# Kernel optimization log

Hardware: AMD Instinct MI355X
Metric: run time of the kernel (lower is better)

The kernel has to match this reference:

```python
import jax, jax.numpy as jnp
import numpy as np

D_MODEL = 1024
N_HEADS = 16
DEPTH = D_MODEL // N_HEADS
NEG_INF = -1.0e9


def setup_inputs() -> dict:
    key = jax.random.key(0)
    ks = jax.random.split(key, 11)
    B, S = 2, 2048
    xk = jax.random.normal(ks[0], (B, S, D_MODEL), jnp.float32)
    xq = jax.random.normal(ks[1], (B, S, D_MODEL), jnp.float32)
    xv = jax.random.normal(ks[2], (B, S, D_MODEL), jnp.float32)
    sc = 1.0 / np.sqrt(D_MODEL)
    wq = jax.random.normal(ks[3], (D_MODEL, D_MODEL), jnp.float32) * sc
    wk = jax.random.normal(ks[4], (D_MODEL, D_MODEL), jnp.float32) * sc
    wv = jax.random.normal(ks[5], (D_MODEL, D_MODEL), jnp.float32) * sc
    wo = jax.random.normal(ks[6], (D_MODEL, D_MODEL), jnp.float32) * sc
    bq = jnp.zeros((D_MODEL,), jnp.float32)
    bk = jnp.zeros((D_MODEL,), jnp.float32)
    bv = jnp.zeros((D_MODEL,), jnp.float32)
    bo = jnp.zeros((D_MODEL,), jnp.float32)
    return {"xk": xk, "xq": xq, "xv": xv, "wq": wq, "bq": bq, "wk": wk,
            "bk": bk, "wv": wv, "bv": bv, "wo": wo, "bo": bo}


def _split_heads(t):
    # [B, S, D] -> [B, H, S, depth]
    B, S, _ = t.shape
    return t.reshape(B, S, N_HEADS, DEPTH).transpose(0, 2, 1, 3)


def reference(xk, xq, xv, wq, bq, wk, bk, wv, bv, wo, bo):
    B, Sq, _ = xq.shape
    Sk = xk.shape[1]
    q = _split_heads(xq @ wq + bq)  # [B,H,Sq,d]
    k = _split_heads(xk @ wk + bk)  # [B,H,Sk,d]
    v = _split_heads(xv @ wv + bv)  # [B,H,Sk,d]
    logits = jnp.einsum('bhqd,bhkd->bhqk', q, k) / jnp.sqrt(
        jnp.asarray(DEPTH, q.dtype))
    # additive causal mask: (1 - lower_triangular) * -1e9
    causal = (1.0 - jnp.tril(jnp.ones((Sq, Sk), logits.dtype))) * NEG_INF
    logits = logits + causal[None, None, :, :]
    attn = jax.nn.softmax(logits, axis=-1)
    out = jnp.einsum('bhqk,bhkd->bhqd', attn, v)
    out = out.transpose(0, 2, 1, 3).reshape(B, Sq, D_MODEL)
    return out @ wo + bo
```

## Files before the change

### kernel.cpp

```cpp
#include <hip/hip_runtime.h>

typedef unsigned short u16;
typedef unsigned int u32;
typedef u16 u16x8 __attribute__((ext_vector_type(8)));
typedef u32 u32x2 __attribute__((ext_vector_type(2)));
typedef __bf16 bf16x8 __attribute__((ext_vector_type(8)));
typedef float f32x4 __attribute__((ext_vector_type(4)));

#define DM 1024
#define SEQ 2048
#define BATCH 2
#define MROWS 4096

__device__ __forceinline__ u16 f2bf(float f) {
  unsigned int x = __builtin_bit_cast(unsigned int, f);
  x += 0x7fffu + ((x >> 16) & 1u);
  return (u16)(x >> 16);
}

__device__ __forceinline__ u32 pack2bf(float lo, float hi) {
  return __builtin_amdgcn_perm(__builtin_bit_cast(u32, hi),
                               __builtin_bit_cast(u32, lo), 0x07060302u);
}

__device__ __forceinline__ void gld16(const void* g, void* l) {
  __builtin_amdgcn_global_load_lds(
      (const __attribute__((address_space(1))) void*)g,
      (__attribute__((address_space(3))) void*)l, 16, 0, 0);
}

struct TrArgs { const float* in[4]; u16* out[4]; };

__global__ __launch_bounds__(256) void transpose_w4(TrArgs a) {
  const float* __restrict__ in = a.in[blockIdx.z];
  u16* __restrict__ out = a.out[blockIdx.z];
  __shared__ u16 T[64][72];
  int r0 = blockIdx.y * 64, c0 = blockIdx.x * 64;
  int t = threadIdx.x;
  int r = t >> 3, cg = (t & 7) * 8;
#pragma unroll
  for (int p = 0; p < 2; p++) {
    const float* src = in + (size_t)(r0 + r + p * 32) * DM + c0 + cg;
    f32x4 x0 = *(const f32x4*)src;
    f32x4 x1 = *(const f32x4*)(src + 4);
    u16x8 v;
#pragma unroll
    for (int j = 0; j < 4; j++) { v[j] = f2bf(x0[j]); v[4 + j] = f2bf(x1[j]); }
    *(u16x8*)(&T[r + p * 32][cg]) = v;
  }
  __syncthreads();
#pragma unroll
  for (int p = 0; p < 2; p++) {
    int orow = r + p * 32;
    u16x8 v;
#pragma unroll
    for (int j = 0; j < 8; j++) v[j] = T[cg + j][orow];
    *(u16x8*)(out + (size_t)(c0 + orow) * DM + r0 + cg) = v;
  }
}

struct CastArgs { const float* in[3]; u16* out[3]; };

__global__ __launch_bounds__(256) void cast_x(CastArgs a) {
  const float* __restrict__ in = a.in[blockIdx.y];
  u16* __restrict__ out = a.out[blockIdx.y];
  size_t e = ((size_t)blockIdx.x * 256 + threadIdx.x) * 8;
  f32x4 a0 = *(const f32x4*)(in + e);
  f32x4 a1 = *(const f32x4*)(in + e + 4);
  u16x8 v;
#pragma unroll
  for (int j = 0; j < 4; j++) { v[j] = f2bf(a0[j]); v[4 + j] = f2bf(a1[j]); }
  *(u16x8*)(out + e) = v;
}

struct GemmArgs { const void* A[3]; const u16* WT[3]; const float* bias[3]; void* C[3]; };

template <int MT, int NT, int BK, bool AF32, bool OF32, bool VT>
__global__ __launch_bounds__(256) void gemmT(GemmArgs g) {
  constexpr int CH = BK / 8;
  constexpr int CM = CH - 1;
  constexpr int SH = (CH == 4) ? 1 : 0;
  __shared__ __align__(16) u16 As[MT * 32 * BK];
  __shared__ __align__(16) u16 Bs[NT * 32 * BK];
  const int z = blockIdx.z;
  const u16* __restrict__ WT = g.WT[z];
  const int tid = threadIdx.x, lane = tid & 63, wave = tid >> 6;
  const int fr = lane & 15, kq = lane >> 4;
  const int mq = (wave >> 1) * (MT * 16), nq = (wave & 1) * (NT * 16);
  const int m0 = blockIdx.y * (MT * 32), n0 = blockIdx.x * (NT * 32);
  const int fsel = (fr >> SH) & CM;
  f32x4 acc[MT][NT] = {};

  for (int kk = 0; kk < DM; kk += BK) {
    __syncthreads();
    constexpr int AI = MT * 32 * CH / 256;
    constexpr int BI = NT * 32 * CH / 256;
    if constexpr (AF32) {
      const float* A = (const float*)g.A[z];
#pragma unroll
      for (int i = 0; i < AI; i++) {
        int ci = i * 256 + tid, row = ci / CH, sl = ci % CH;
        int sc = (sl ^ ((row >> SH) & CM)) * 8;
        const float* s0 = A + (size_t)(m0 + row) * DM + kk + sc;
        f32x4 a0 = *(const f32x4*)s0, a1 = *(const f32x4*)(s0 + 4);
        u16x8 v;
#pragma unroll
        for (int j = 0; j < 4; j++) { v[j] = f2bf(a0[j]); v[4 + j] = f2bf(a1[j]); }
        *(u16x8*)(As + ci * 8) = v;
      }
    } else {
      const u16* A = (const u16*)g.A[z];
#pragma unroll
      for (int i = 0; i < AI; i++) {
        int ci = i * 256 + tid, row = ci / CH, sl = ci % CH;
        int sc = (sl ^ ((row >> SH) & CM)) * 8;
        gld16(A + (size_t)(m0 + row) * DM + kk + sc, As + ci * 8);
      }
    }
#pragma unroll
    for (int i = 0; i < BI; i++) {
      int ci = i * 256 + tid, row = ci / CH, sl = ci % CH;
      int sc = (sl ^ ((row >> SH) & CM)) * 8;
      gld16(WT + (size_t)(n0 + row) * DM + kk + sc, Bs + ci * 8);
    }
    __syncthreads();
#pragma unroll
    for (int kc = 0; kc < BK / 32; kc++) {
      bf16x8 af[MT], bfr[NT];
      const int fo = ((kc * 4 + kq) ^ fsel) * 8;
#pragma unroll
      for (int mt = 0; mt < MT; mt++)
        af[mt] = __builtin_bit_cast(
            bf16x8, *(const u16x8*)(As + (mq + mt * 16 + fr) * BK + fo));
#pragma unroll
      for (int nt = 0; nt < NT; nt++)
        bfr[nt] = __builtin_bit_cast(
            bf16x8, *(const u16x8*)(Bs + (nq + nt * 16 + fr) * BK + fo));
#pragma unroll
      for (int mt = 0; mt < MT; mt++)
#pragma unroll
        for (int nt = 0; nt < NT; nt++)
          acc[mt][nt] = __builtin_amdgcn_mfma_f32_16x16x32_bf16(
              af[mt], bfr[nt], acc[mt][nt], 0, 0, 0);
    }
  }
  const float* __restrict__ bias = g.bias[z];
  const bool vtr = VT && (z == 2);
#pragma unroll
  for (int nt = 0; nt < NT; nt++) {
    int col = n0 + nq + nt * 16 + fr;
    float bb = bias[col];
#pragma unroll
    for (int mt = 0; mt < MT; mt++)
#pragma unroll
      for (int r = 0; r < 4; r++) {
        int row = m0 + mq + mt * 16 + kq * 4 + r;
        float val = acc[mt][nt][r] + bb;
        if constexpr (OF32) {
          ((float*)g.C[z])[(size_t)row * DM + col] = val;
        } else {
          u16* C = (u16*)g.C[z];
          if (vtr) {
            size_t idx = ((size_t)((row >> 11) * 16 + (col >> 6)) * 64 +
                          (col & 63)) * SEQ + (row & 2047);
            C[idx] = f2bf(val);
          } else {
            C[(size_t)row * DM + col] = f2bf(val);
          }
        }
      }
  }
}

__global__ __launch_bounds__(128) void attn4(u16* __restrict__ Q,
                                             const u16* __restrict__ K,
                                             const u16* __restrict__ Vtg) {
  __shared__ __align__(16) u16 Ksh[64 * 64];
  __shared__ __align__(16) u16 Vsh[64 * 64];
  __shared__ __align__(16) u16 Psh[64 * 64];
  __shared__ float Lbuf[2][32];
  const int tid = threadIdx.x, wq = tid >> 6, lane = tid & 63;
  const int fr = lane & 15, kq = lane >> 4, f7 = fr & 7;
  const int bh = blockIdx.x, b = bh >> 4, h = bh & 15;
  const int qt = 31 - blockIdx.y;
  const float C1 = 0.125f * 1.44269504f;

  int xo[2];
  xo[0] = (kq ^ f7) * 8;
  xo[1] = ((4 + kq) ^ f7) * 8;

  const u16* kp[4];
  const u16* vp[4];
#pragma unroll
  for (int i = 0; i < 4; i++) {
    int ci = i * 128 + tid, row = ci >> 3, sl = ci & 7;
    int sc = (sl ^ (row & 7)) * 8;
    kp[i] = K + (size_t)(b * SEQ + row) * DM + h * 64 + sc;
    vp[i] = Vtg + (size_t)(bh * 64 + row) * SEQ + sc;
  }

  bf16x8 qf[2][2];
#pragma unroll
  for (int qtl = 0; qtl < 2; qtl++) {
    size_t qr = (size_t)(b * SEQ + qt * 64 + wq * 32 + qtl * 16 + fr) * DM + h * 64;
#pragma unroll
    for (int kk = 0; kk < 2; kk++)
      qf[qtl][kk] =
          __builtin_bit_cast(bf16x8, *(const u16x8*)(Q + qr + kk * 32 + kq * 8));
  }

  f32x4 ov[2][4] = {};
  float lac[2] = {0.f, 0.f};

  for (int t = 0; t <= qt; t++) {
    __syncthreads();
#pragma unroll
    for (int i = 0; i < 4; i++) {
      int ci = i * 128 + tid;
      gld16(kp[i] + (size_t)t * 64 * DM, Ksh + ci * 8);
      gld16(vp[i] + t * 64, Vsh + ci * 8);
    }
    __syncthreads();

    f32x4 st[2][4];
#pragma unroll
    for (int kt = 0; kt < 4; kt++) {
      bf16x8 k0 = __builtin_bit_cast(
          bf16x8, *(const u16x8*)(Ksh + (kt * 16 + fr) * 64 + xo[0]));
      bf16x8 k1 = __builtin_bit_cast(
          bf16x8, *(const u16x8*)(Ksh + (kt * 16 + fr) * 64 + xo[1]));
#pragma unroll
      for (int qtl = 0; qtl < 2; qtl++) {
        f32x4 s = {};
        s = __builtin_amdgcn_mfma_f32_16x16x32_bf16(k0, qf[qtl][0], s, 0, 0, 0);
        s = __builtin_amdgcn_mfma_f32_16x16x32_bf16(k1, qf[qtl][1], s, 0, 0, 0);
        st[qtl][kt] = s;
      }
    }
    if (t == qt) {
#pragma unroll
      for (int qtl = 0; qtl < 2; qtl++)
#pragma unroll
        for (int kt = 0; kt < 4; kt++)
#pragma unroll
          for (int r = 0; r < 4; r++)
            if (kt * 16 + kq * 4 + r > wq * 32 + qtl * 16 + fr)
              st[qtl][kt][r] = -1e30f;
    }
#pragma unroll
    for (int qtl = 0; qtl < 2; qtl++) {
      float ls = 0.f;
      int prow = (wq * 32 + qtl * 16 + fr) * 64;
#pragma unroll
      for (int kt = 0; kt < 4; kt++) {
        float p0 = __builtin_amdgcn_exp2f(st[qtl][kt][0] * C1);
        float p1 = __builtin_amdgcn_exp2f(st[qtl][kt][1] * C1);
        float p2 = __builtin_amdgcn_exp2f(st[qtl][kt][2] * C1);
        float p3 = __builtin_amdgcn_exp2f(st[qtl][kt][3] * C1);
        ls += (p0 + p1) + (p2 + p3);
        u32x2 d;
        d[0] = pack2bf(p0, p1);
        d[1] = pack2bf(p2, p3);
        int sl = (2 * kt + (kq >> 1)) ^ f7;
        *(u32x2*)(Psh + prow + sl * 8 + (kq & 1) * 4) = d;
      }
      ls += __shfl_xor(ls, 16);
      ls += __shfl_xor(ls, 32);
      lac[qtl] += ls;
    }
#pragma unroll
    for (int kk = 0; kk < 2; kk++) {
      bf16x8 pa[2];
#pragma unroll
      for (int qtl = 0; qtl < 2; qtl++)
        pa[qtl] = __builtin_bit_cast(
            bf16x8,
            *(const u16x8*)(Psh + (wq * 32 + qtl * 16 + fr) * 64 + xo[kk]));
#pragma unroll
      for (int nt = 0; nt < 4; nt++) {
        bf16x8 vb = __builtin_bit_cast(
            bf16x8, *(const u16x8*)(Vsh + (nt * 16 + fr) * 64 + xo[kk]));
#pragma unroll
        for (int qtl = 0; qtl < 2; qtl++)
          ov[qtl][nt] = __builtin_amdgcn_mfma_f32_16x16x32_bf16(
              pa[qtl], vb, ov[qtl][nt], 0, 0, 0);
      }
    }
  }
  if (kq == 0) {
    Lbuf[wq][fr] = lac[0];
    Lbuf[wq][16 + fr] = lac[1];
  }
#pragma unroll
  for (int qtl = 0; qtl < 2; qtl++) {
    float rinv[4];
#pragma unroll
    for (int r = 0; r < 4; r++)
      rinv[r] = 1.0f / Lbuf[wq][qtl * 16 + kq * 4 + r];
#pragma unroll
    for (int nt = 0; nt < 4; nt++)
#pragma unroll
      for (int r = 0; r < 4; r++) {
        int row = qt * 64 + wq * 32 + qtl * 16 + kq * 4 + r;
        Q[(size_t)(b * SEQ + row) * DM + h * 64 + nt * 16 + fr] =
            f2bf(ov[qtl][nt][r] * rinv[r]);
      }
  }
}

extern "C" void kernel_launch(void* const* d_in, const int* in_sizes, int n_in,
                              void* d_out, int out_size, void* d_ws,
                              size_t ws_size, hipStream_t stream) {
  const float* xk = (const float*)d_in[0];
  const float* xq = (const float*)d_in[1];
  const float* xv = (const float*)d_in[2];
  const float* wq = (const float*)d_in[3];
  const float* bq = (const float*)d_in[4];
  const float* wk = (const float*)d_in[5];
  const float* bk = (const float*)d_in[6];
  const float* wv = (const float*)d_in[7];
  const float* bv = (const float*)d_in[8];
  const float* wo = (const float*)d_in[9];
  const float* bo = (const float*)d_in[10];

  u16* Qb = (u16*)d_ws;
  u16* Kb = Qb + (size_t)MROWS * DM;
  u16* Vb = Kb + (size_t)MROWS * DM;
  u16* WTq = Vb + (size_t)MROWS * DM;
  u16* WTk = WTq + (size_t)DM * DM;
  u16* WTv = WTk + (size_t)DM * DM;
  u16* WTo = WTv + (size_t)DM * DM;
  u16* Xq = WTo + (size_t)DM * DM;
  u16* Xk = Xq + (size_t)MROWS * DM;
  u16* Xv = Xk + (size_t)MROWS * DM;
  const bool cast_path =
      ws_size >= ((size_t)(3 * 8 + 4 * 2 + 3 * 8)) * 1024 * 1024;

  dim3 blk(256);

  TrArgs tr;
  tr.in[0] = wq; tr.in[1] = wk; tr.in[2] = wv; tr.in[3] = wo;
  tr.out[0] = WTq; tr.out[1] = WTk; tr.out[2] = WTv; tr.out[3] = WTo;
  transpose_w4<<<dim3(16, 16, 4), blk, 0, stream>>>(tr);

  GemmArgs gq;
  gq.WT[0] = WTq; gq.WT[1] = WTk; gq.WT[2] = WTv;
  gq.bias[0] = bq; gq.bias[1] = bk; gq.bias[2] = bv;
  gq.C[0] = Qb; gq.C[1] = Kb; gq.C[2] = Vb;
  if (cast_path) {
    CastArgs ca;
    ca.in[0] = xq; ca.in[1] = xk; ca.in[2] = xv;
    ca.out[0] = Xq; ca.out[1] = Xk; ca.out[2] = Xv;
    cast_x<<<dim3(MROWS * DM / 2048, 3), blk, 0, stream>>>(ca);
    gq.A[0] = Xq; gq.A[1] = Xk; gq.A[2] = Xv;
    gemmT<4, 4, 64, false, false, true>
        <<<dim3(DM / 128, MROWS / 128, 3), blk, 0, stream>>>(gq);
  } else {
    gq.A[0] = xq; gq.A[1] = xk; gq.A[2] = xv;
    gemmT<4, 4, 64, true, false, true>
        <<<dim3(DM / 128, MROWS / 128, 3), blk, 0, stream>>>(gq);
  }

  attn4<<<dim3(BATCH * 16, 32), dim3(128), 0, stream>>>(Qb, Kb, Vb);

  GemmArgs go;
  go.A[0] = Qb; go.WT[0] = WTo; go.bias[0] = bo; go.C[0] = d_out;
  go.A[1] = Qb; go.WT[1] = WTo; go.bias[1] = bo; go.C[1] = d_out;
  go.A[2] = Qb; go.WT[2] = WTo; go.bias[2] = bo; go.C[2] = d_out;
  gemmT<2, 2, 64, false, true, false>
      <<<dim3(DM / 64, MROWS / 64, 1), blk, 0, stream>>>(go);
}
```

Before: 240.9 us.

## Double-buffer LDS in GEMM and attention, fuse input cast, widen out-proj tile

Both the projection GEMM and the attention kernel now use two LDS buffers, so the next K-step (or next K/V tile) is loaded while MFMAs run on the current one. Each iteration now needs only one barrier instead of two. The separate fp32-to-bf16 cast kernel is removed, and the QKV GEMM converts fp32 inputs directly while staging them. The transposed V store is packed into 8-byte writes, and the output projection moves to a 2x4 tile. The risks are the extra LDS use and a smaller K step (32), and the fp32 A staging stays synchronous, so less of its load latency can be hidden.

```diff
diff --git a/kernel.cpp b/kernel.cpp
--- a/kernel.cpp
+++ b/kernel.cpp
@@ -17,7 +17,9 @@
   x += 0x7fffu + ((x >> 16) & 1u);
   return (u16)(x >> 16);
 }
-
+__device__ __forceinline__ u32 f2bf2(float lo, float hi) {
+  return (u32)f2bf(lo) | ((u32)f2bf(hi) << 16);
+}
 __device__ __forceinline__ u32 pack2bf(float lo, float hi) {
   return __builtin_amdgcn_perm(__builtin_bit_cast(u32, hi),
                                __builtin_bit_cast(u32, lo), 0x07060302u);
@@ -59,91 +61,76 @@
   }
 }
 
-struct CastArgs { const float* in[3]; u16* out[3]; };
-
-__global__ __launch_bounds__(256) void cast_x(CastArgs a) {
-  const float* __restrict__ in = a.in[blockIdx.y];
-  u16* __restrict__ out = a.out[blockIdx.y];
-  size_t e = ((size_t)blockIdx.x * 256 + threadIdx.x) * 8;
-  f32x4 a0 = *(const f32x4*)(in + e);
-  f32x4 a1 = *(const f32x4*)(in + e + 4);
-  u16x8 v;
-#pragma unroll
-  for (int j = 0; j < 4; j++) { v[j] = f2bf(a0[j]); v[4 + j] = f2bf(a1[j]); }
-  *(u16x8*)(out + e) = v;
-}
-
 struct GemmArgs { const void* A[3]; const u16* WT[3]; const float* bias[3]; void* C[3]; };
 
-template <int MT, int NT, int BK, bool AF32, bool OF32, bool VT>
+template <int MT, int NT, bool AF32, bool OF32, bool VT>
 __global__ __launch_bounds__(256) void gemmT(GemmArgs g) {
-  constexpr int CH = BK / 8;
-  constexpr int CM = CH - 1;
-  constexpr int SH = (CH == 4) ? 1 : 0;
-  __shared__ __align__(16) u16 As[MT * 32 * BK];
-  __shared__ __align__(16) u16 Bs[NT * 32 * BK];
+  __shared__ __align__(16) u16 As[2][MT * 32 * 32];
+  __shared__ __align__(16) u16 Bs[2][NT * 32 * 32];
   const int z = blockIdx.z;
   const u16* __restrict__ WT = g.WT[z];
   const int tid = threadIdx.x, lane = tid & 63, wave = tid >> 6;
   const int fr = lane & 15, kq = lane >> 4;
   const int mq = (wave >> 1) * (MT * 16), nq = (wave & 1) * (NT * 16);
   const int m0 = blockIdx.y * (MT * 32), n0 = blockIdx.x * (NT * 32);
-  const int fsel = (fr >> SH) & CM;
+  const int fo = ((kq ^ ((fr >> 1) & 3)) * 8);
+  constexpr int AI = MT / 2, BI = NT / 2;
   f32x4 acc[MT][NT] = {};
 
-  for (int kk = 0; kk < DM; kk += BK) {
-    __syncthreads();
-    constexpr int AI = MT * 32 * CH / 256;
-    constexpr int BI = NT * 32 * CH / 256;
+  auto stage = [&](int buf, int kk) {
     if constexpr (AF32) {
       const float* A = (const float*)g.A[z];
 #pragma unroll
       for (int i = 0; i < AI; i++) {
-        int ci = i * 256 + tid, row = ci / CH, sl = ci % CH;
-        int sc = (sl ^ ((row >> SH) & CM)) * 8;
+        int ci = i * 256 + tid, row = ci >> 2, sl = ci & 3;
+        int sc = (sl ^ ((row >> 1) & 3)) * 8;
         const float* s0 = A + (size_t)(m0 + row) * DM + kk + sc;
         f32x4 a0 = *(const f32x4*)s0, a1 = *(const f32x4*)(s0 + 4);
         u16x8 v;
 #pragma unroll
         for (int j = 0; j < 4; j++) { v[j] = f2bf(a0[j]); v[4 + j] = f2bf(a1[j]); }
-        *(u16x8*)(As + ci * 8) = v;
+        *(u16x8*)(As[buf] + ci * 8) = v;
       }
     } else {
       const u16* A = (const u16*)g.A[z];
 #pragma unroll
       for (int i = 0; i < AI; i++) {
-        int ci = i * 256 + tid, row = ci / CH, sl = ci % CH;
-        int sc = (sl ^ ((row >> SH) & CM)) * 8;
-        gld16(A + (size_t)(m0 + row) * DM + kk + sc, As + ci * 8);
+        int ci = i * 256 + tid, row = ci >> 2, sl = ci & 3;
+        int sc = (sl ^ ((row >> 1) & 3)) * 8;
+        gld16(A + (size_t)(m0 + row) * DM + kk + sc, As[buf] + ci * 8);
       }
     }
 #pragma unroll
     for (int i = 0; i < BI; i++) {
-      int ci = i * 256 + tid, row = ci / CH, sl = ci % CH;
-      int sc = (sl ^ ((row >> SH) & CM)) * 8;
-      gld16(WT + (size_t)(n0 + row) * DM + kk + sc, Bs + ci * 8);
-    }
+      int ci = i * 256 + tid, row = ci >> 2, sl = ci & 3;
+      int sc = (sl ^ ((row >> 1) & 3)) * 8;
+      gld16(WT + (size_t)(n0 + row) * DM + kk + sc, Bs[buf] + ci * 8);
+    }
+  };
+
+  stage(0, 0);
+  __syncthreads();
+  for (int k = 0; k < DM / 32; k++) {
+    if (k + 1 < DM / 32) stage((k + 1) & 1, (k + 1) * 32);
+    const int buf = k & 1;
+    bf16x8 af[MT], bfr[NT];
+#pragma unroll
+    for (int mt = 0; mt < MT; mt++)
+      af[mt] = __builtin_bit_cast(
+          bf16x8, *(const u16x8*)(As[buf] + (mq + mt * 16 + fr) * 32 + fo));
+#pragma unroll
+    for (int nt = 0; nt < NT; nt++)
+      bfr[nt] = __builtin_bit_cast(
+          bf16x8, *(const u16x8*)(Bs[buf] + (nq + nt * 16 + fr) * 32 + fo));
+#pragma unroll
+    for (int mt = 0; mt < MT; mt++)
+#pragma unroll
+      for (int nt = 0; nt < NT; nt++)
+        acc[mt][nt] = __builtin_amdgcn_mfma_f32_16x16x32_bf16(
+            af[mt], bfr[nt], acc[mt][nt], 0, 0, 0);
     __syncthreads();
-#pragma unroll
-    for (int kc = 0; kc < BK / 32; kc++) {
-      bf16x8 af[MT], bfr[NT];
-      const int fo = ((kc * 4 + kq) ^ fsel) * 8;
-#pragma unroll
-      for (int mt = 0; mt < MT; mt++)
-        af[mt] = __builtin_bit_cast(
-            bf16x8, *(const u16x8*)(As + (mq + mt * 16 + fr) * BK + fo));
-#pragma unroll
-      for (int nt = 0; nt < NT; nt++)
-        bfr[nt] = __builtin_bit_cast(
-            bf16x8, *(const u16x8*)(Bs + (nq + nt * 16 + fr) * BK + fo));
-#pragma unroll
-      for (int mt = 0; mt < MT; mt++)
-#pragma unroll
-        for (int nt = 0; nt < NT; nt++)
-          acc[mt][nt] = __builtin_amdgcn_mfma_f32_16x16x32_bf16(
-              af[mt], bfr[nt], acc[mt][nt], 0, 0, 0);
-    }
-  }
+  }
+
   const float* __restrict__ bias = g.bias[z];
   const bool vtr = VT && (z == 2);
 #pragma unroll
@@ -151,32 +138,34 @@
     int col = n0 + nq + nt * 16 + fr;
     float bb = bias[col];
 #pragma unroll
-    for (int mt = 0; mt < MT; mt++)
-#pragma unroll
-      for (int r = 0; r < 4; r++) {
-        int row = m0 + mq + mt * 16 + kq * 4 + r;
-        float val = acc[mt][nt][r] + bb;
-        if constexpr (OF32) {
-          ((float*)g.C[z])[(size_t)row * DM + col] = val;
-        } else {
-          u16* C = (u16*)g.C[z];
-          if (vtr) {
-            size_t idx = ((size_t)((row >> 11) * 16 + (col >> 6)) * 64 +
-                          (col & 63)) * SEQ + (row & 2047);
-            C[idx] = f2bf(val);
-          } else {
-            C[(size_t)row * DM + col] = f2bf(val);
-          }
+    for (int mt = 0; mt < MT; mt++) {
+      int row0 = m0 + mq + mt * 16 + kq * 4;
+      if (vtr) {
+        u32x2 d;
+        d[0] = f2bf2(acc[mt][nt][0] + bb, acc[mt][nt][1] + bb);
+        d[1] = f2bf2(acc[mt][nt][2] + bb, acc[mt][nt][3] + bb);
+        size_t idx = ((size_t)((row0 >> 11) * 16 + (col >> 6)) * 64 +
+                      (col & 63)) * SEQ + (row0 & 2047);
+        *(u32x2*)((u16*)g.C[z] + idx) = d;
+      } else {
+#pragma unroll
+        for (int r = 0; r < 4; r++) {
+          float val = acc[mt][nt][r] + bb;
+          if constexpr (OF32)
+            ((float*)g.C[z])[(size_t)(row0 + r) * DM + col] = val;
+          else
+            ((u16*)g.C[z])[(size_t)(row0 + r) * DM + col] = f2bf(val);
         }
       }
-  }
-}
-
-__global__ __launch_bounds__(128) void attn4(u16* __restrict__ Q,
+    }
+  }
+}
+
+__global__ __launch_bounds__(128) void attn5(u16* __restrict__ Q,
                                              const u16* __restrict__ K,
                                              const u16* __restrict__ Vtg) {
-  __shared__ __align__(16) u16 Ksh[64 * 64];
-  __shared__ __align__(16) u16 Vsh[64 * 64];
+  __shared__ __align__(16) u16 Ksh[2][64 * 64];
+  __shared__ __align__(16) u16 Vsh[2][64 * 64];
   __shared__ __align__(16) u16 Psh[64 * 64];
   __shared__ float Lbuf[2][32];
   const int tid = threadIdx.x, wq = tid >> 6, lane = tid & 63;
@@ -198,6 +187,14 @@
     kp[i] = K + (size_t)(b * SEQ + row) * DM + h * 64 + sc;
     vp[i] = Vtg + (size_t)(bh * 64 + row) * SEQ + sc;
   }
+  auto stage = [&](int buf, int t) {
+#pragma unroll
+    for (int i = 0; i < 4; i++) {
+      int ci = i * 128 + tid;
+      gld16(kp[i] + (size_t)t * 64 * DM, Ksh[buf] + ci * 8);
+      gld16(vp[i] + t * 64, Vsh[buf] + ci * 8);
+    }
+  };
 
   bf16x8 qf[2][2];
 #pragma unroll
@@ -212,23 +209,19 @@
   f32x4 ov[2][4] = {};
   float lac[2] = {0.f, 0.f};
 
+  stage(0, 0);
+  __syncthreads();
   for (int t = 0; t <= qt; t++) {
-    __syncthreads();
-#pragma unroll
-    for (int i = 0; i < 4; i++) {
-      int ci = i * 128 + tid;
-      gld16(kp[i] + (size_t)t * 64 * DM, Ksh + ci * 8);
-      gld16(vp[i] + t * 64, Vsh + ci * 8);
-    }
-    __syncthreads();
+    if (t < qt) stage((t + 1) & 1, t + 1);
+    const int buf = t & 1;
 
     f32x4 st[2][4];
 #pragma unroll
     for (int kt = 0; kt < 4; kt++) {
       bf16x8 k0 = __builtin_bit_cast(
-          bf16x8, *(const u16x8*)(Ksh + (kt * 16 + fr) * 64 + xo[0]));
+          bf16x8, *(const u16x8*)(Ksh[buf] + (kt * 16 + fr) * 64 + xo[0]));
       bf16x8 k1 = __builtin_bit_cast(
-          bf16x8, *(const u16x8*)(Ksh + (kt * 16 + fr) * 64 + xo[1]));
+          bf16x8, *(const u16x8*)(Ksh[buf] + (kt * 16 + fr) * 64 + xo[1]));
 #pragma unroll
       for (int qtl = 0; qtl < 2; qtl++) {
         f32x4 s = {};
@@ -279,13 +272,14 @@
 #pragma unroll
       for (int nt = 0; nt < 4; nt++) {
         bf16x8 vb = __builtin_bit_cast(
-            bf16x8, *(const u16x8*)(Vsh + (nt * 16 + fr) * 64 + xo[kk]));
+            bf16x8, *(const u16x8*)(Vsh[buf] + (nt * 16 + fr) * 64 + xo[kk]));
 #pragma unroll
         for (int qtl = 0; qtl < 2; qtl++)
           ov[qtl][nt] = __builtin_amdgcn_mfma_f32_16x16x32_bf16(
               pa[qtl], vb, ov[qtl][nt], 0, 0, 0);
       }
     }
+    __syncthreads();
   }
   if (kq == 0) {
     Lbuf[wq][fr] = lac[0];
@@ -330,11 +324,6 @@
   u16* WTk = WTq + (size_t)DM * DM;
   u16* WTv = WTk + (size_t)DM * DM;
   u16* WTo = WTv + (size_t)DM * DM;
-  u16* Xq = WTo + (size_t)DM * DM;
-  u16* Xk = Xq + (size_t)MROWS * DM;
-  u16* Xv = Xk + (size_t)MROWS * DM;
-  const bool cast_path =
-      ws_size >= ((size_t)(3 * 8 + 4 * 2 + 3 * 8)) * 1024 * 1024;
 
   dim3 blk(256);
 
@@ -344,29 +333,19 @@
   transpose_w4<<<dim3(16, 16, 4), blk, 0, stream>>>(tr);
 
   GemmArgs gq;
+  gq.A[0] = xq; gq.A[1] = xk; gq.A[2] = xv;
   gq.WT[0] = WTq; gq.WT[1] = WTk; gq.WT[2] = WTv;
   gq.bias[0] = bq; gq.bias[1] = bk; gq.bias[2] = bv;
   gq.C[0] = Qb; gq.C[1] = Kb; gq.C[2] = Vb;
-  if (cast_path) {
-    CastArgs ca;
-    ca.in[0] = xq; ca.in[1] = xk; ca.in[2] = xv;
-    ca.out[0] = Xq; ca.out[1] = Xk; ca.out[2] = Xv;
-    cast_x<<<dim3(MROWS * DM / 2048, 3), blk, 0, stream>>>(ca);
-    gq.A[0] = Xq; gq.A[1] = Xk; gq.A[2] = Xv;
-    gemmT<4, 4, 64, false, false, true>
-        <<<dim3(DM / 128, MROWS / 128, 3), blk, 0, stream>>>(gq);
-  } else {
-    gq.A[0] = xq; gq.A[1] = xk; gq.A[2] = xv;
-    gemmT<4, 4, 64, true, false, true>
-        <<<dim3(DM / 128, MROWS / 128, 3), blk, 0, stream>>>(gq);
-  }
-
-  attn4<<<dim3(BATCH * 16, 32), dim3(128), 0, stream>>>(Qb, Kb, Vb);
+  gemmT<4, 4, true, false, true>
+      <<<dim3(DM / 128, MROWS / 128, 3), blk, 0, stream>>>(gq);
+
+  attn5<<<dim3(BATCH * 16, 32), dim3(128), 0, stream>>>(Qb, Kb, Vb);
 
   GemmArgs go;
   go.A[0] = Qb; go.WT[0] = WTo; go.bias[0] = bo; go.C[0] = d_out;
   go.A[1] = Qb; go.WT[1] = WTo; go.bias[1] = bo; go.C[1] = d_out;
   go.A[2] = Qb; go.WT[2] = WTo; go.bias[2] = bo; go.C[2] = d_out;
-  gemmT<2, 2, 64, false, true, false>
-      <<<dim3(DM / 64, MROWS / 64, 1), blk, 0, stream>>>(go);
-}
+  gemmT<2, 4, false, true, false>
+      <<<dim3(DM / 128, MROWS / 64, 1), blk, 0, stream>>>(go);
+}
```

After: 237.5 us. About the same (-1.4%).
